# Kernel optimization log

Hardware: AMD Instinct MI355X
Metric: run time of the kernel (lower is better)

Reference implementation:

```python
import jax, jax.numpy as jnp
import numpy as np
from jax.scipy.special import gammaln

BIG_NEG = -1e9
MAX_K = 20  # args.sm_max_span_length


def setup_inputs() -> dict:
    key = jax.random.key(0)
    ks = jax.random.split(key, 7)
    B, N, d, C = 16, 2048, 256, 128
    features = jax.random.normal(ks[0], (B, N, d), dtype=jnp.float32)
    lengths = jax.random.randint(ks[1], (B,), N // 2, N + 1)
    gaussian_means = jax.random.normal(ks[2], (C, d), dtype=jnp.float32)
    cov_diag = jax.random.uniform(ks[3], (d,), minval=0.5, maxval=1.5, dtype=jnp.float32)
    transition_logits = jax.random.normal(ks[4], (C, C), dtype=jnp.float32)
    init_logits = jax.random.uniform(ks[5], (C,), dtype=jnp.float32)
    poisson_log_rates = jax.random.normal(ks[6], (C,), dtype=jnp.float32) * 0.5 + 1.5
    return {"features": features, "lengths": lengths, "gaussian_means": gaussian_means,
            "cov_diag": cov_diag, "transition_logits": transition_logits,
            "init_logits": init_logits, "poisson_log_rates": poisson_log_rates}


def _emission_log_probs(features, means, cov_diag):
    # Diagonal-covariance MultivariateNormal log-prob, one class per column.
    # Quadratic form expanded to avoid materializing [B,N,C,d].
    inv_var = 1.0 / cov_diag
    d = features.shape[-1]
    const = -0.5 * (d * jnp.log(2.0 * jnp.pi) + jnp.sum(jnp.log(cov_diag)))
    xq = jnp.einsum('bnd,d->bn', features * features, inv_var)          # [B,N]
    mq = jnp.einsum('cd,d->c', means * means, inv_var)                  # [C]
    xm = jnp.einsum('bnd,cd->bnc', features, means * inv_var)           # [B,N,C]
    return const - 0.5 * (xq[..., None] + mq[None, None, :] - 2.0 * xm)  # [B,N,C]


def _length_log_probs(log_rates, K):
    # Poisson log-prob for span lengths k = 1..K.
    ks = jnp.arange(1, K + 1, dtype=jnp.float32)[:, None]               # [K,1]
    return ks * log_rates[None, :] - jnp.exp(log_rates)[None, :] - gammaln(ks + 1.0)  # [K,C]


def _transition_log_probs(transition_logits):
    C = transition_logits.shape[0]
    masked = jnp.where(jnp.eye(C, dtype=bool), BIG_NEG, transition_logits)  # no self-transitions
    return jax.nn.log_softmax(masked, axis=0)  # normalized over destination class (dim 0)


def _semimarkov_logZ(emis_lp, lengths, init_lp, trans_lp, len_lp, K):
    # Segmental (semi-Markov) CRF forward algorithm with sliding-window span sums.
    B, N, C = emis_lp.shape
    cum = jnp.concatenate([jnp.zeros((B, 1, C), emis_lp.dtype), jnp.cumsum(emis_lp, axis=1)], axis=1)
    cum_pad = jnp.concatenate([jnp.zeros((B, K, C), emis_lp.dtype), cum], axis=1)  # idx t+K <-> position t
    beta0 = jnp.full((B, N + 1 + K, C), BIG_NEG, emis_lp.dtype)
    beta0 = beta0.at[:, K, :].set(init_lp[None, :])  # position 0: initial distribution
    len_rev = len_lp[::-1]  # len_rev[j] == length log-prob of span length K-j

    def step(beta, t):
        w = jax.lax.dynamic_slice(beta, (0, t, 0), (B, K, C))        # beta at positions t-K..t-1
        cw = jax.lax.dynamic_slice(cum_pad, (0, t, 0), (B, K, C))
        ct = jax.lax.dynamic_slice(cum_pad, (0, t + K, 0), (B, 1, C))
        span = w + len_rev[None, :, :] + (ct - cw)                    # [B,K,C] span scores ending at t
        alpha_t = jax.nn.logsumexp(span, axis=1)                      # [B,C]
        beta_t = jax.nn.logsumexp(alpha_t[:, None, :] + trans_lp[None, :, :], axis=2)  # to-class
        beta = jax.lax.dynamic_update_slice(beta, beta_t[:, None, :], (0, t + K, 0))
        return beta, alpha_t

    _, alphas = jax.lax.scan(step, beta0, jnp.arange(1, N + 1))       # alphas: [N,B,C]
    final = alphas[lengths - 1, jnp.arange(B)]                        # [B,C] at each sequence end
    return jax.nn.logsumexp(final, axis=1)                            # [B] log partition


def reference(features, lengths, gaussian_means, cov_diag, transition_logits, init_logits, poisson_log_rates):
    emis_lp = _emission_log_probs(features, gaussian_means, cov_diag)
    init_lp = jax.nn.log_softmax(init_logits, axis=0)
    trans_lp = _transition_log_probs(transition_logits)
    len_lp = _length_log_probs(poisson_log_rates, MAX_K)
    return _semimarkov_logZ(emis_lp, lengths, init_lp, trans_lp, len_lp, MAX_K)
```

## Files before the change

kernel.cpp:

```cpp
#include <hip/hip_runtime.h>
#include <math.h>

#define Bb 16
#define Nn 2048
#define Dd 256
#define Cc 128
#define Kk 20
#define BIG_NEG -1.0e9f

#define WS_EMIS   0
#define WS_MSC    (WS_EMIS + Bb*Nn*Cc)
#define WS_XQ     (WS_MSC + Cc*Dd)
#define WS_ECHAN  (WS_XQ + Bb*Nn)
#define WS_T      (WS_ECHAN + Cc)
#define WS_LEN    (WS_T + Cc*Cc)
#define WS_INIT   (WS_LEN + Kk*Cc)
#define WS_IVAR   (WS_INIT + Cc)

typedef __attribute__((ext_vector_type(8))) short short8;
typedef __attribute__((ext_vector_type(4))) float float4v;

__device__ __forceinline__ unsigned short f32_to_bf16(float x) {
  unsigned int u = __builtin_bit_cast(unsigned int, x);
  u = (u + 0x7FFFu + ((u >> 16) & 1u)) >> 16;
  return (unsigned short)u;
}

#define DPP_STEP(x, op, ctrl, rmask)                                          \
  do {                                                                        \
    int _yi = __builtin_amdgcn_update_dpp(                                    \
        __builtin_bit_cast(int, x), __builtin_bit_cast(int, x), ctrl, rmask,  \
        0xF, true);                                                           \
    x = op(x, __builtin_bit_cast(float, _yi));                                \
  } while (0)

__device__ __forceinline__ float dpp_add(float a, float b) { return a + b; }

__device__ __forceinline__ float wave_max64(float x) {
  DPP_STEP(x, fmaxf, 0xB1, 0xF);
  DPP_STEP(x, fmaxf, 0x4E, 0xF);
  DPP_STEP(x, fmaxf, 0x141, 0xF);
  DPP_STEP(x, fmaxf, 0x140, 0xF);
  DPP_STEP(x, fmaxf, 0x142, 0xA);
  DPP_STEP(x, fmaxf, 0x143, 0xC);
  return __builtin_bit_cast(float,
      __builtin_amdgcn_readlane(__builtin_bit_cast(int, x), 63));
}

__device__ __forceinline__ float wave_sum64(float x) {
  DPP_STEP(x, dpp_add, 0xB1, 0xF);
  DPP_STEP(x, dpp_add, 0x4E, 0xF);
  DPP_STEP(x, dpp_add, 0x141, 0xF);
  DPP_STEP(x, dpp_add, 0x140, 0xF);
  DPP_STEP(x, dpp_add, 0x142, 0xA);
  DPP_STEP(x, dpp_add, 0x143, 0xC);
  return __builtin_bit_cast(float,
      __builtin_amdgcn_readlane(__builtin_bit_cast(int, x), 63));
}

__global__ void prep_kernel(const float* __restrict__ means,
                            const float* __restrict__ cov,
                            const float* __restrict__ tl,
                            const float* __restrict__ il,
                            const float* __restrict__ plr,
                            float* __restrict__ ws) {
  __shared__ float s_iv[Dd];
  __shared__ float s_red[4];
  __shared__ float s_tlse[Cc];
  int tid = threadIdx.x;

  float cv = cov[tid];
  float iv = 1.0f / cv;
  s_iv[tid] = iv;
  ws[WS_IVAR + tid] = iv;
  float lg = __logf(cv);
  #pragma unroll
  for (int off = 1; off < 64; off <<= 1) lg += __shfl_xor(lg, off, 64);
  if ((tid & 63) == 0) s_red[tid >> 6] = lg;
  __syncthreads();
  float logdet = s_red[0] + s_red[1] + s_red[2] + s_red[3];
  float cconst = -0.5f * ((float)Dd * 1.8378770664093453f + logdet);

  for (int idx = tid; idx < Cc * Dd; idx += 256) {
    int d = idx & (Dd - 1);
    ws[WS_MSC + idx] = means[idx] * s_iv[d];
  }
  if (tid < Cc) {
    float acc = 0.0f;
    for (int d = 0; d < Dd; d++) {
      float m = means[tid * Dd + d];
      acc = fmaf(m * m, s_iv[d], acc);
    }
    ws[WS_ECHAN + tid] = cconst - 0.5f * acc;
  }
  for (int idx = tid; idx < Kk * Cc; idx += 256) {
    int L = idx / Cc + 1;
    int c = idx & (Cc - 1);
    float r = plr[c];
    ws[WS_LEN + idx] = (float)L * r - __expf(r) - lgammaf((float)(L + 1));
  }

  __syncthreads();
  float x = (tid < Cc) ? il[tid] : -INFINITY;
  float mx = x;
  #pragma unroll
  for (int off = 1; off < 64; off <<= 1) mx = fmaxf(mx, __shfl_xor(mx, off, 64));
  if ((tid & 63) == 0) s_red[tid >> 6] = mx;
  __syncthreads();
  float M = fmaxf(s_red[0], s_red[1]);
  float se = (tid < Cc) ? __expf(x - M) : 0.0f;
  #pragma unroll
  for (int off = 1; off < 64; off <<= 1) se += __shfl_xor(se, off, 64);
  __syncthreads();
  if ((tid & 63) == 0) s_red[tid >> 6] = se;
  __syncthreads();
  float lse = M + __logf(s_red[0] + s_red[1]);
  if (tid < Cc) ws[WS_INIT + tid] = x - lse;

  if (tid < Cc) {
    int j = tid;
    float m2 = -INFINITY;
    for (int i = 0; i < Cc; i++) if (i != j) m2 = fmaxf(m2, tl[i * Cc + j]);
    float s2 = 0.0f;
    for (int i = 0; i < Cc; i++) if (i != j) s2 += __expf(tl[i * Cc + j] - m2);
    s_tlse[j] = m2 + __logf(s2);
  }
  __syncthreads();
  for (int idx = tid; idx < Cc * Cc; idx += 256) {
    int i = idx / Cc;
    int j = idx & (Cc - 1);
    ws[WS_T + idx] = (i == j) ? 0.0f : __expf(tl[idx] - s_tlse[j]);
  }
}

__global__ void xq_kernel(const float* __restrict__ f, float* __restrict__ ws) {
  int pos = blockIdx.x * 4 + (threadIdx.x >> 6);
  int lane = threadIdx.x & 63;
  const float4 fv = *(const float4*)&f[(size_t)pos * Dd + lane * 4];
  const float4 vv = *(const float4*)&ws[WS_IVAR + lane * 4];
  float a = fv.x * fv.x * vv.x + fv.y * fv.y * vv.y +
            fv.z * fv.z * vv.z + fv.w * fv.w * vv.w;
  #pragma unroll
  for (int off = 1; off < 64; off <<= 1) a += __shfl_xor(a, off, 64);
  if (lane == 0) ws[WS_XQ + pos] = a;
}

__global__ void emis_kernel(const float* __restrict__ f, float* __restrict__ ws) {
  __shared__ float fA[32][32];
  __shared__ float msT[32][Cc];
  const float* msc = ws + WS_MSC;
  float* emis = ws + WS_EMIS;
  int tid = threadIdx.x;
  int b = blockIdx.x >> 6;
  int n0 = (blockIdx.x & 63) << 5;
  int c = tid & (Cc - 1), g = tid >> 7;
  float acc[16];
  #pragma unroll
  for (int i = 0; i < 16; i++) acc[i] = 0.0f;

  for (int d0 = 0; d0 < Dd; d0 += 32) {
    int row = tid >> 3, col = (tid & 7) << 2;
    *(float4*)&fA[row][col] =
        *(const float4*)&f[(size_t)(b * Nn + n0 + row) * Dd + d0 + col];
    int cc = tid & 127, dd0 = (tid >> 7) << 4;
    float4 v0 = *(const float4*)&msc[cc * Dd + d0 + dd0];
    float4 v1 = *(const float4*)&msc[cc * Dd + d0 + dd0 + 4];
    float4 v2 = *(const float4*)&msc[cc * Dd + d0 + dd0 + 8];
    float4 v3 = *(const float4*)&msc[cc * Dd + d0 + dd0 + 12];
    msT[dd0 + 0][cc] = v0.x; msT[dd0 + 1][cc] = v0.y;
    msT[dd0 + 2][cc] = v0.z; msT[dd0 + 3][cc] = v0.w;
    msT[dd0 + 4][cc] = v1.x; msT[dd0 + 5][cc] = v1.y;
    msT[dd0 + 6][cc] = v1.z; msT[dd0 + 7][cc] = v1.w;
    msT[dd0 + 8][cc] = v2.x; msT[dd0 + 9][cc] = v2.y;
    msT[dd0 + 10][cc] = v2.z; msT[dd0 + 11][cc] = v2.w;
    msT[dd0 + 12][cc] = v3.x; msT[dd0 + 13][cc] = v3.y;
    msT[dd0 + 14][cc] = v3.z; msT[dd0 + 15][cc] = v3.w;
    __syncthreads();
    #pragma unroll
    for (int dd = 0; dd < 32; dd++) {
      float mv = msT[dd][c];
      #pragma unroll
      for (int n = 0; n < 16; n++)
        acc[n] = fmaf(fA[g * 16 + n][dd], mv, acc[n]);
    }
    __syncthreads();
  }
  float ec = ws[WS_ECHAN + c];
  #pragma unroll
  for (int n = 0; n < 16; n++) {
    int nn = n0 + g * 16 + n;
    emis[(size_t)(b * Nn + nn) * Cc + c] = ec - 0.5f * ws[WS_XQ + b * Nn + nn] + acc[n];
  }
}

__launch_bounds__(128, 1)
__global__ void scan_kernel(const int* __restrict__ lengths,
                            const float* __restrict__ ws,
                            float* __restrict__ out) {
  __shared__ __align__(16) unsigned short lds_pb[2][Cc];
  __shared__ float lds_wmax[2][2];
  __shared__ float lds_ps[2];
  int tid = threadIdx.x;
  int b = blockIdx.x;
  int c = tid;
  int w = tid >> 6;
  int lane = tid & 63;
  int g = lane >> 4;
  int len_b = lengths[b];
  const float* emis = ws + WS_EMIS + (size_t)b * Nn * Cc;

  short8 Tf[4][4];
  {
    const float* T = ws + WS_T;
    int row_lo = w * 64 + (lane & 15);
    int kg = g * 8;
    #pragma unroll
    for (int nt = 0; nt < 4; nt++)
      #pragma unroll
      for (int kt = 0; kt < 4; kt++) {
        const float* src = &T[(size_t)(row_lo + nt * 16) * Cc + kt * 32 + kg];
        short8 fr;
        #pragma unroll
        for (int j = 0; j < 8; j++) fr[j] = (short)f32_to_bf16(src[j]);
        Tf[nt][kt] = fr;
      }
  }

  float lenv[Kk];
  #pragma unroll
  for (int i = 0; i < Kk; i++) lenv[i] = ws[WS_LEN + i * Cc + c];
  float len0 = lenv[0];
  float dlen[Kk - 1];
  #pragma unroll
  for (int i = 1; i < Kk; i++) dlen[i - 1] = lenv[i] - lenv[i - 1];

  float h[Kk];
  #pragma unroll
  for (int i = 0; i < Kk; i++) h[i] = BIG_NEG;
  h[0] = ws[WS_INIT + c] + len0;

  float cum = emis[0 * Cc + c];
  float e[8], en[8];
  #pragma unroll
  for (int i = 0; i < 8; i++) e[i] = emis[(size_t)(1 + i) * Cc + c];

  bool done = false;
  for (int tg = 1; tg <= Nn && !done; tg += 8) {
    #pragma unroll
    for (int i = 0; i < 8; i++) {
      int r = tg + 8 + i; if (r > Nn - 1) r = Nn - 1;
      en[i] = emis[(size_t)r * Cc + c];
    }
    #pragma unroll
    for (int i = 0; i < 8; i++) {
      int t = tg + i;
      int buf = t & 1;

      float m2[10];
      #pragma unroll
      for (int k = 0; k < 9; k++) m2[k] = fmaxf(h[1 + 2 * k], h[2 + 2 * k]);
      m2[9] = h[19];
      float m4a = fmaxf(fmaxf(m2[0], m2[1]), fmaxf(m2[2], m2[3]));
      float m4b = fmaxf(fmaxf(m2[4], m2[5]), fmaxf(m2[6], m2[7]));
      float m19 = fmaxf(fmaxf(m4a, m4b), fmaxf(m2[8], m2[9]));
      float mloc = fmaxf(m19, h[0]);
      float mabs = mloc + cum;
      float wm = wave_max64(mabs);

      float ex[Kk];
      #pragma unroll
      for (int k = 0; k < Kk; k++) ex[k] = __expf(h[k] - mloc);
      float s4[5];
      #pragma unroll
      for (int k = 0; k < 5; k++)
        s4[k] = (ex[4 * k] + ex[4 * k + 1]) + (ex[4 * k + 2] + ex[4 * k + 3]);
      float s = ((s4[0] + s4[1]) + (s4[2] + s4[3])) + s4[4];

      float p = s * __expf(mabs - wm);
      lds_pb[buf][c] = f32_to_bf16(p);
      if (lane == 0) lds_wmax[buf][w] = wm;
      bool is_out = (t == len_b);
      if (is_out) {
        float ps = wave_sum64(p);
        if (lane == 0) lds_ps[w] = ps;
      }
      __syncthreads();

      float MA = lds_wmax[buf][0], MB = lds_wmax[buf][1];
      float Mt = fmaxf(MA, MB);
      float sA = __expf(MA - Mt), sB = __expf(MB - Mt);

      const unsigned short* pb = lds_pb[buf];
      short8 pa[4];
      #pragma unroll
      for (int kt = 0; kt < 4; kt++)
        pa[kt] = *(const short8*)&pb[kt * 32 + g * 8];

      float4v accA[4], accB[4];
      #pragma unroll
      for (int nt = 0; nt < 4; nt++) {
        float4v z = {0.0f, 0.0f, 0.0f, 0.0f};
        accA[nt] = __builtin_amdgcn_mfma_f32_16x16x32_bf16(pa[1], Tf[nt][1],
                     __builtin_amdgcn_mfma_f32_16x16x32_bf16(pa[0], Tf[nt][0], z, 0, 0, 0),
                     0, 0, 0);
        accB[nt] = __builtin_amdgcn_mfma_f32_16x16x32_bf16(pa[3], Tf[nt][3],
                     __builtin_amdgcn_mfma_f32_16x16x32_bf16(pa[2], Tf[nt][2], z, 0, 0, 0),
                     0, 0, 0);
      }
      float qa0 = (g == 0) ? accA[0][0] : accA[1][0];
      float qa1 = (g == 2) ? accA[2][0] : accA[3][0];
      float qa = (g < 2) ? qa0 : qa1;
      float qb0 = (g == 0) ? accB[0][0] : accB[1][0];
      float qb1 = (g == 2) ? accB[2][0] : accB[3][0];
      float qb = (g < 2) ? qb0 : qb1;
      float q = qa * sA + qb * sB;

      float rel = cum - Mt;
      float gnew = (q > 0.0f) ? (__logf(q) - rel) : (-80.0f - rel);

      if (is_out) {
        if (tid == 0) out[b] = Mt + __logf(lds_ps[0] * sA + lds_ps[1] * sB);
        done = true;
        break;
      }

      #pragma unroll
      for (int k = Kk - 1; k > 0; k--) h[k] = h[k - 1] + dlen[k - 1];
      h[0] = gnew + len0;
      cum += e[i];
    }
    if (!done) {
      #pragma unroll
      for (int i = 0; i < 8; i++) e[i] = en[i];
    }
  }
}

extern "C" void kernel_launch(void* const* d_in, const int* in_sizes, int n_in,
                              void* d_out, int out_size, void* d_ws, size_t ws_size,
                              hipStream_t stream) {
  const float* features = (const float*)d_in[0];
  const int* lengths = (const int*)d_in[1];
  const float* means = (const float*)d_in[2];
  const float* cov = (const float*)d_in[3];
  const float* tl = (const float*)d_in[4];
  const float* il = (const float*)d_in[5];
  const float* plr = (const float*)d_in[6];
  float* out = (float*)d_out;
  float* ws = (float*)d_ws;

  prep_kernel<<<1, 256, 0, stream>>>(means, cov, tl, il, plr, ws);
  xq_kernel<<<(Bb * Nn) / 4, 256, 0, stream>>>(features, ws);
  emis_kernel<<<Bb * (Nn / 32), 256, 0, stream>>>(features, ws);
  scan_kernel<<<Bb, 128, 0, stream>>>(lengths, ws, out);
}
```

Before: 1.700 ms.

## Move emission GEMM to bf16 MFMA and overlap scan span sums with the barrier

The emission matmul now runs on bf16 MFMA instructions, with features converted on the fly and scaled means stored as bf16, in place of the scalar FP32 LDS-tiled loop. In the scan, the logsumexp over the 19 older span slots is computed after the barrier, alongside the transition MFMAs, and carried into the next step. Only the fresh slot is combined before the barrier, which shortens the serial critical path per timestep. The costs are lower precision in the emission scores and more complex scan state carried across steps.

```diff
diff --git a/kernel.cpp b/kernel.cpp
--- a/kernel.cpp
+++ b/kernel.cpp
@@ -81,9 +81,10 @@
   float logdet = s_red[0] + s_red[1] + s_red[2] + s_red[3];
   float cconst = -0.5f * ((float)Dd * 1.8378770664093453f + logdet);
 
+  unsigned short* mscb = (unsigned short*)(ws + WS_MSC);
   for (int idx = tid; idx < Cc * Dd; idx += 256) {
     int d = idx & (Dd - 1);
-    ws[WS_MSC + idx] = means[idx] * s_iv[d];
+    mscb[idx] = f32_to_bf16(means[idx] * s_iv[d]);
   }
   if (tid < Cc) {
     float acc = 0.0f;
@@ -145,51 +146,63 @@
   if (lane == 0) ws[WS_XQ + pos] = a;
 }
 
-__global__ void emis_kernel(const float* __restrict__ f, float* __restrict__ ws) {
-  __shared__ float fA[32][32];
-  __shared__ float msT[32][Cc];
-  const float* msc = ws + WS_MSC;
+__launch_bounds__(256)
+__global__ void emis_mfma_kernel(const float* __restrict__ f, float* __restrict__ ws) {
+  const unsigned short* msc = (const unsigned short*)(ws + WS_MSC);
   float* emis = ws + WS_EMIS;
   int tid = threadIdx.x;
+  int w = tid >> 6, lane = tid & 63, g = lane >> 4, l16 = lane & 15;
   int b = blockIdx.x >> 6;
   int n0 = (blockIdx.x & 63) << 5;
-  int c = tid & (Cc - 1), g = tid >> 7;
-  float acc[16];
-  #pragma unroll
-  for (int i = 0; i < 16; i++) acc[i] = 0.0f;
-
-  for (int d0 = 0; d0 < Dd; d0 += 32) {
-    int row = tid >> 3, col = (tid & 7) << 2;
-    *(float4*)&fA[row][col] =
-        *(const float4*)&f[(size_t)(b * Nn + n0 + row) * Dd + d0 + col];
-    int cc = tid & 127, dd0 = (tid >> 7) << 4;
-    float4 v0 = *(const float4*)&msc[cc * Dd + d0 + dd0];
-    float4 v1 = *(const float4*)&msc[cc * Dd + d0 + dd0 + 4];
-    float4 v2 = *(const float4*)&msc[cc * Dd + d0 + dd0 + 8];
-    float4 v3 = *(const float4*)&msc[cc * Dd + d0 + dd0 + 12];
-    msT[dd0 + 0][cc] = v0.x; msT[dd0 + 1][cc] = v0.y;
-    msT[dd0 + 2][cc] = v0.z; msT[dd0 + 3][cc] = v0.w;
-    msT[dd0 + 4][cc] = v1.x; msT[dd0 + 5][cc] = v1.y;
-    msT[dd0 + 6][cc] = v1.z; msT[dd0 + 7][cc] = v1.w;
-    msT[dd0 + 8][cc] = v2.x; msT[dd0 + 9][cc] = v2.y;
-    msT[dd0 + 10][cc] = v2.z; msT[dd0 + 11][cc] = v2.w;
-    msT[dd0 + 12][cc] = v3.x; msT[dd0 + 13][cc] = v3.y;
-    msT[dd0 + 14][cc] = v3.z; msT[dd0 + 15][cc] = v3.w;
-    __syncthreads();
-    #pragma unroll
-    for (int dd = 0; dd < 32; dd++) {
-      float mv = msT[dd][c];
-      #pragma unroll
-      for (int n = 0; n < 16; n++)
-        acc[n] = fmaf(fA[g * 16 + n][dd], mv, acc[n]);
-    }
-    __syncthreads();
-  }
-  float ec = ws[WS_ECHAN + c];
-  #pragma unroll
-  for (int n = 0; n < 16; n++) {
-    int nn = n0 + g * 16 + n;
-    emis[(size_t)(b * Nn + nn) * Cc + c] = ec - 0.5f * ws[WS_XQ + b * Nn + nn] + acc[n];
+  int c0 = w << 5;
+
+  const float* fbase = f + (size_t)(b * Nn + n0) * Dd;
+  float4v acc[2][2];
+  #pragma unroll
+  for (int rt = 0; rt < 2; rt++)
+    #pragma unroll
+    for (int ct = 0; ct < 2; ct++) acc[rt][ct] = (float4v){0.f, 0.f, 0.f, 0.f};
+
+  #pragma unroll
+  for (int k0 = 0; k0 < Dd; k0 += 32) {
+    int kk = k0 + g * 8;
+    short8 afr[2], bfr[2];
+    #pragma unroll
+    for (int rt = 0; rt < 2; rt++) {
+      const float* src = fbase + (size_t)(rt * 16 + l16) * Dd + kk;
+      float4 v0 = *(const float4*)src;
+      float4 v1 = *(const float4*)(src + 4);
+      short8 fr;
+      fr[0] = (short)f32_to_bf16(v0.x); fr[1] = (short)f32_to_bf16(v0.y);
+      fr[2] = (short)f32_to_bf16(v0.z); fr[3] = (short)f32_to_bf16(v0.w);
+      fr[4] = (short)f32_to_bf16(v1.x); fr[5] = (short)f32_to_bf16(v1.y);
+      fr[6] = (short)f32_to_bf16(v1.z); fr[7] = (short)f32_to_bf16(v1.w);
+      afr[rt] = fr;
+    }
+    #pragma unroll
+    for (int ct = 0; ct < 2; ct++)
+      bfr[ct] = *(const short8*)&msc[(size_t)(c0 + ct * 16 + l16) * Dd + kk];
+    #pragma unroll
+    for (int rt = 0; rt < 2; rt++)
+      #pragma unroll
+      for (int ct = 0; ct < 2; ct++)
+        acc[rt][ct] = __builtin_amdgcn_mfma_f32_16x16x32_bf16(afr[rt], bfr[ct], acc[rt][ct], 0, 0, 0);
+  }
+
+  #pragma unroll
+  for (int rt = 0; rt < 2; rt++) {
+    #pragma unroll
+    for (int ct = 0; ct < 2; ct++) {
+      int cc = c0 + ct * 16 + l16;
+      float ec = ws[WS_ECHAN + cc];
+      #pragma unroll
+      for (int r = 0; r < 4; r++) {
+        int row = rt * 16 + g * 4 + r;
+        int nn = n0 + row;
+        emis[(size_t)(b * Nn + nn) * Cc + cc] =
+            ec - 0.5f * ws[WS_XQ + b * Nn + nn] + acc[rt][ct][r];
+      }
+    }
   }
 }
 
@@ -237,7 +250,10 @@
   float h[Kk];
   #pragma unroll
   for (int i = 0; i < Kk; i++) h[i] = BIG_NEG;
-  h[0] = ws[WS_INIT + c] + len0;
+
+  float gnew = ws[WS_INIT + c];
+  float pm = BIG_NEG;
+  float ps = 19.0f;
 
   float cum = emis[0 * Cc + c];
   float e[8], en[8];
@@ -246,60 +262,65 @@
 
   bool done = false;
   for (int tg = 1; tg <= Nn && !done; tg += 8) {
-    #pragma unroll
-    for (int i = 0; i < 8; i++) {
-      int r = tg + 8 + i; if (r > Nn - 1) r = Nn - 1;
-      en[i] = emis[(size_t)r * Cc + c];
-    }
     #pragma unroll
     for (int i = 0; i < 8; i++) {
       int t = tg + i;
       int buf = t & 1;
 
+      float h0 = gnew + len0;
+      float m = fmaxf(pm, h0);
+      float sfix = fmaf(ps, __expf(pm - m), __expf(h0 - m));
+      float mabs = m + cum;
+      float wm = wave_max64(mabs);
+      float p = sfix * __expf(mabs - wm);
+      lds_pb[buf][c] = f32_to_bf16(p);
+      if (lane == 0) lds_wmax[buf][w] = wm;
+      bool is_out = (t == len_b);
+      if (is_out) {
+        float pssum = wave_sum64(p);
+        if (lane == 0) lds_ps[w] = pssum;
+      }
+      h[0] = h0;
+      __syncthreads();
+
+      if (i == 0) {
+        #pragma unroll
+        for (int j = 0; j < 8; j++) {
+          int r = tg + 8 + j; if (r > Nn - 1) r = Nn - 1;
+          en[j] = emis[(size_t)r * Cc + c];
+        }
+      }
+      float MA = lds_wmax[buf][0], MB = lds_wmax[buf][1];
+      const unsigned short* pb = lds_pb[buf];
+      short8 pa[4];
+      #pragma unroll
+      for (int kt = 0; kt < 4; kt++)
+        pa[kt] = *(const short8*)&pb[kt * 32 + g * 8];
+
+      #pragma unroll
+      for (int k = Kk - 1; k > 0; k--) h[k] = h[k - 1] + dlen[k - 1];
       float m2[10];
       #pragma unroll
       for (int k = 0; k < 9; k++) m2[k] = fmaxf(h[1 + 2 * k], h[2 + 2 * k]);
       m2[9] = h[19];
       float m4a = fmaxf(fmaxf(m2[0], m2[1]), fmaxf(m2[2], m2[3]));
       float m4b = fmaxf(fmaxf(m2[4], m2[5]), fmaxf(m2[6], m2[7]));
-      float m19 = fmaxf(fmaxf(m4a, m4b), fmaxf(m2[8], m2[9]));
-      float mloc = fmaxf(m19, h[0]);
-      float mabs = mloc + cum;
-      float wm = wave_max64(mabs);
-
-      float ex[Kk];
-      #pragma unroll
-      for (int k = 0; k < Kk; k++) ex[k] = __expf(h[k] - mloc);
+      float pm2 = fmaxf(fmaxf(m4a, m4b), fmaxf(m2[8], m2[9]));
+      float ex[Kk - 1];
+      #pragma unroll
+      for (int k = 1; k < Kk; k++) ex[k - 1] = __expf(h[k] - pm2);
       float s4[5];
-      #pragma unroll
-      for (int k = 0; k < 5; k++)
-        s4[k] = (ex[4 * k] + ex[4 * k + 1]) + (ex[4 * k + 2] + ex[4 * k + 3]);
-      float s = ((s4[0] + s4[1]) + (s4[2] + s4[3])) + s4[4];
-
-      float p = s * __expf(mabs - wm);
-      lds_pb[buf][c] = f32_to_bf16(p);
-      if (lane == 0) lds_wmax[buf][w] = wm;
-      bool is_out = (t == len_b);
-      if (is_out) {
-        float ps = wave_sum64(p);
-        if (lane == 0) lds_ps[w] = ps;
-      }
-      __syncthreads();
-
-      float MA = lds_wmax[buf][0], MB = lds_wmax[buf][1];
-      float Mt = fmaxf(MA, MB);
-      float sA = __expf(MA - Mt), sB = __expf(MB - Mt);
-
-      const unsigned short* pb = lds_pb[buf];
-      short8 pa[4];
-      #pragma unroll
-      for (int kt = 0; kt < 4; kt++)
-        pa[kt] = *(const short8*)&pb[kt * 32 + g * 8];
-
+      s4[0] = (ex[0] + ex[1]) + (ex[2] + ex[3]);
+      s4[1] = (ex[4] + ex[5]) + (ex[6] + ex[7]);
+      s4[2] = (ex[8] + ex[9]) + (ex[10] + ex[11]);
+      s4[3] = (ex[12] + ex[13]) + (ex[14] + ex[15]);
+      s4[4] = (ex[16] + ex[17]) + ex[18];
+      float ps2 = ((s4[0] + s4[1]) + (s4[2] + s4[3])) + s4[4];
+
+      float4v z = {0.0f, 0.0f, 0.0f, 0.0f};
       float4v accA[4], accB[4];
       #pragma unroll
       for (int nt = 0; nt < 4; nt++) {
-        float4v z = {0.0f, 0.0f, 0.0f, 0.0f};
         accA[nt] = __builtin_amdgcn_mfma_f32_16x16x32_bf16(pa[1], Tf[nt][1],
                      __builtin_amdgcn_mfma_f32_16x16x32_bf16(pa[0], Tf[nt][0], z, 0, 0, 0),
                      0, 0, 0);
@@ -307,6 +328,8 @@
                      __builtin_amdgcn_mfma_f32_16x16x32_bf16(pa[2], Tf[nt][2], z, 0, 0, 0),
                      0, 0, 0);
       }
+      float Mt = fmaxf(MA, MB);
+      float sA = __expf(MA - Mt), sB = __expf(MB - Mt);
       float qa0 = (g == 0) ? accA[0][0] : accA[1][0];
       float qa1 = (g == 2) ? accA[2][0] : accA[3][0];
       float qa = (g < 2) ? qa0 : qa1;
@@ -316,17 +339,15 @@
       float q = qa * sA + qb * sB;
 
       float rel = cum - Mt;
-      float gnew = (q > 0.0f) ? (__logf(q) - rel) : (-80.0f - rel);
+      gnew = (q > 0.0f) ? (__logf(q) - rel) : (-80.0f - rel);
 
       if (is_out) {
         if (tid == 0) out[b] = Mt + __logf(lds_ps[0] * sA + lds_ps[1] * sB);
         done = true;
         break;
       }
-
-      #pragma unroll
-      for (int k = Kk - 1; k > 0; k--) h[k] = h[k - 1] + dlen[k - 1];
-      h[0] = gnew + len0;
+      pm = pm2;
+      ps = ps2;
       cum += e[i];
     }
     if (!done) {
@@ -351,6 +372,6 @@
 
   prep_kernel<<<1, 256, 0, stream>>>(means, cov, tl, il, plr, ws);
   xq_kernel<<<(Bb * Nn) / 4, 256, 0, stream>>>(features, ws);
-  emis_kernel<<<Bb * (Nn / 32), 256, 0, stream>>>(features, ws);
+  emis_mfma_kernel<<<Bb * (Nn / 32), 256, 0, stream>>>(features, ws);
   scan_kernel<<<Bb, 128, 0, stream>>>(lengths, ws, out);
 }
```

After: 1.541 ms. 9.4% less time.
